# Optimization experiments

Measured on AMD Instinct MI355X. Metric: run time of the kernel, lower is better.

The kernel has to match this reference:

```python
import jax, jax.numpy as jnp
import numpy as np


def setup_inputs() -> dict:
    key = jax.random.key(0)
    k1, k2, k3 = jax.random.split(key, 3)
    x = jax.random.normal(k1, (8, 256, 160, 160), dtype=jnp.float32)
    # conv weights: OIHW layout, Kaiming-ish scale
    w7 = jax.random.normal(k2, (1, 2, 7, 7), dtype=jnp.float32) * (1.0 / np.sqrt(2 * 7 * 7))
    w3 = jax.random.normal(k3, (1, 2, 3, 3), dtype=jnp.float32) * (1.0 / np.sqrt(2 * 3 * 3))
    alpha = jnp.asarray(0.5, dtype=jnp.float32)
    return {"x": x, "w7": w7, "w3": w3, "alpha": alpha}


def _conv_same(desc, w, pad):
    # desc: [B, 2, H, W], w: [1, 2, k, k] -> [B, 1, H, W]
    return jax.lax.conv_general_dilated(
        desc, w, window_strides=(1, 1), padding=[(pad, pad), (pad, pad)],
        dimension_numbers=("NCHW", "OIHW", "NCHW"))


def reference(x, w7, w3, alpha):
    avg = jnp.mean(x, axis=1, keepdims=True)          # [B,1,H,W]
    mx = jnp.max(x, axis=1, keepdims=True)            # [B,1,H,W]
    desc = jnp.concatenate([avg, mx], axis=1)         # [B,2,H,W]
    a7 = _conv_same(desc, w7, 3)
    a3 = _conv_same(desc, w3, 1)
    w = jax.nn.sigmoid(alpha * a7 + (1.0 - alpha) * a3)
    return x * w
```

## Files before the change

kernel.cpp:

```cpp
#include <hip/hip_runtime.h>
#include <float.h>
#include <math.h>

#define Bn 8
#define Cn 256
#define Hn 160
#define Wn 160
#define HWn (Hn * Wn)
#define NPIX (Bn * HWn)
#define NTOT (Bn * Cn * HWn)
#define PBLK 256
#define BLKS (NPIX / PBLK)
#define BPB  (HWn / PBLK)

typedef float v4f __attribute__((ext_vector_type(4)));

__global__ __launch_bounds__(256) void k_reduce(const float* __restrict__ x,
                                                float* __restrict__ avgp,
                                                float* __restrict__ maxp) {
    const int tid  = threadIdx.x;
    const int lane = tid & 63;
    const int wv   = tid >> 6;
    const int base = blockIdx.x << 8;
    const int b    = base / HWn;
    const int hwb  = base - b * HWn;
    const float* xp = x + (size_t)b * Cn * HWn + hwb + (lane << 2);
    const int c0 = wv << 6;

    float4 s = make_float4(0.f, 0.f, 0.f, 0.f);
    float4 m = make_float4(-FLT_MAX, -FLT_MAX, -FLT_MAX, -FLT_MAX);
    #pragma unroll 8
    for (int c = 0; c < 64; ++c) {
        const float4 v = *reinterpret_cast<const float4*>(xp + (size_t)(c0 + c) * HWn);
        s.x += v.x; s.y += v.y; s.z += v.z; s.w += v.w;
        m.x = fmaxf(m.x, v.x); m.y = fmaxf(m.y, v.y);
        m.z = fmaxf(m.z, v.z); m.w = fmaxf(m.w, v.w);
    }

    __shared__ float4 ss[4][64];
    __shared__ float4 sm[4][64];
    ss[wv][lane] = s;
    sm[wv][lane] = m;
    __syncthreads();

    if (tid < 64) {
        const float4 s0 = ss[0][tid], s1 = ss[1][tid], s2 = ss[2][tid], s3 = ss[3][tid];
        const float4 m0 = sm[0][tid], m1 = sm[1][tid], m2 = sm[2][tid], m3 = sm[3][tid];
        const float inv = 1.0f / (float)Cn;
        float4 av, mx;
        av.x = (s0.x + s1.x + s2.x + s3.x) * inv;
        av.y = (s0.y + s1.y + s2.y + s3.y) * inv;
        av.z = (s0.z + s1.z + s2.z + s3.z) * inv;
        av.w = (s0.w + s1.w + s2.w + s3.w) * inv;
        mx.x = fmaxf(fmaxf(m0.x, m1.x), fmaxf(m2.x, m3.x));
        mx.y = fmaxf(fmaxf(m0.y, m1.y), fmaxf(m2.y, m3.y));
        mx.z = fmaxf(fmaxf(m0.z, m1.z), fmaxf(m2.z, m3.z));
        mx.w = fmaxf(fmaxf(m0.w, m1.w), fmaxf(m2.w, m3.w));
        reinterpret_cast<float4*>(avgp)[(base >> 2) + tid] = av;
        reinterpret_cast<float4*>(maxp)[(base >> 2) + tid] = mx;
    }
}

__global__ __launch_bounds__(256) void k_convmul(const float* __restrict__ x,
                                                 const float* __restrict__ avgp,
                                                 const float* __restrict__ maxp,
                                                 const float* __restrict__ w7,
                                                 const float* __restrict__ w3,
                                                 const float* __restrict__ alphap,
                                                 float* __restrict__ out) {
    __shared__ float w_lds[PBLK];

    const int tid  = threadIdx.x;
    const int base = blockIdx.x << 8;
    const int b    = base / HWn;
    const int hwb  = base - b * HWn;

    {
        const int hw = hwb + tid;
        const int h  = hw / Wn;
        const int w  = hw - h * Wn;
        const float* ap = avgp + b * HWn;
        const float* mp = maxp + b * HWn;

        float a7 = 0.f;
        #pragma unroll
        for (int kh = 0; kh < 7; ++kh) {
            const int hh = h + kh - 3;
            if (hh < 0 || hh >= Hn) continue;
            #pragma unroll
            for (int kw = 0; kw < 7; ++kw) {
                const int ww = w + kw - 3;
                if (ww < 0 || ww >= Wn) continue;
                const int o = hh * Wn + ww;
                a7 = fmaf(ap[o], w7[kh * 7 + kw], a7);
                a7 = fmaf(mp[o], w7[49 + kh * 7 + kw], a7);
            }
        }

        float a3 = 0.f;
        #pragma unroll
        for (int kh = 0; kh < 3; ++kh) {
            const int hh = h + kh - 1;
            if (hh < 0 || hh >= Hn) continue;
            #pragma unroll
            for (int kw = 0; kw < 3; ++kw) {
                const int ww = w + kw - 1;
                if (ww < 0 || ww >= Wn) continue;
                const int o = hh * Wn + ww;
                a3 = fmaf(ap[o], w3[kh * 3 + kw], a3);
                a3 = fmaf(mp[o], w3[9 + kh * 3 + kw], a3);
            }
        }

        const float alpha = *alphap;
        const float z = alpha * a7 + (1.0f - alpha) * a3;
        w_lds[tid] = 1.0f / (1.0f + expf(-z));
    }
    __syncthreads();

    const int lane = tid & 63;
    const int wv   = tid >> 6;
    const int c0   = wv << 6;

    const float4 wf = reinterpret_cast<const float4*>(w_lds)[lane];
    const v4f wvf = { wf.x, wf.y, wf.z, wf.w };

    const size_t off0 = (size_t)b * Cn * HWn + hwb + (lane << 2);
    const v4f* __restrict__ xin = reinterpret_cast<const v4f*>(x + off0);
    v4f* __restrict__ oout = reinterpret_cast<v4f*>(out + off0);

    #pragma unroll 8
    for (int c = 0; c < 64; ++c) {
        const size_t idx = ((size_t)(c0 + c) * HWn) >> 2;
        const v4f xv = __builtin_nontemporal_load(xin + idx);
        __builtin_nontemporal_store(xv * wvf, oout + idx);
    }
}

extern "C" void kernel_launch(void* const* d_in, const int* in_sizes, int n_in,
                              void* d_out, int out_size, void* d_ws, size_t ws_size,
                              hipStream_t stream) {
    const float* x      = (const float*)d_in[0];
    const float* w7     = (const float*)d_in[1];
    const float* w3     = (const float*)d_in[2];
    const float* alphap = (const float*)d_in[3];
    float* out = (float*)d_out;

    float* avgp = (float*)d_ws;
    float* maxp = avgp + NPIX;

    k_reduce <<<BLKS, 256, 0, stream>>>(x, avgp, maxp);
    k_convmul<<<BLKS, 256, 0, stream>>>(x, avgp, maxp, w7, w3, alphap, out);
}
```

Baseline: 114.9 us.

## Fuse channel reduction and conv-multiply into one cooperative kernel with grid sync

The two kernels become a single cooperative kernel. Each block first reduces its pixel tile over channels, then waits at a grid-wide barrier, then computes the 7x7/3x3 conv and sigmoid and scales x. The aim is to drop the second kernel launch and its gap, and to re-read each block's x slice while it may still sit in the large last-level cache, so the x load is now a normal load instead of a nontemporal one. In exchange, all 800 blocks must be co-resident for the cooperative launch to work. The grid barrier adds a global synchronisation point that serialises the two phases across the whole device.

```diff
diff --git a/kernel.cpp b/kernel.cpp
--- a/kernel.cpp
+++ b/kernel.cpp
@@ -1,6 +1,9 @@
 #include <hip/hip_runtime.h>
+#include <hip/hip_cooperative_groups.h>
 #include <float.h>
 #include <math.h>
+
+namespace cg = cooperative_groups;
 
 #define Bn 8
 #define Cn 256
@@ -8,73 +11,67 @@
 #define Wn 160
 #define HWn (Hn * Wn)
 #define NPIX (Bn * HWn)
-#define NTOT (Bn * Cn * HWn)
 #define PBLK 256
 #define BLKS (NPIX / PBLK)
-#define BPB  (HWn / PBLK)
 
 typedef float v4f __attribute__((ext_vector_type(4)));
 
-__global__ __launch_bounds__(256) void k_reduce(const float* __restrict__ x,
-                                                float* __restrict__ avgp,
-                                                float* __restrict__ maxp) {
+__global__ __launch_bounds__(256) void k_fused(const float* __restrict__ x,
+                                               const float* __restrict__ w7,
+                                               const float* __restrict__ w3,
+                                               const float* __restrict__ alphap,
+                                               float* __restrict__ avgp,
+                                               float* __restrict__ maxp,
+                                               float* __restrict__ out) {
     const int tid  = threadIdx.x;
     const int lane = tid & 63;
     const int wv   = tid >> 6;
     const int base = blockIdx.x << 8;
     const int b    = base / HWn;
     const int hwb  = base - b * HWn;
-    const float* xp = x + (size_t)b * Cn * HWn + hwb + (lane << 2);
-    const int c0 = wv << 6;
+    const int c0   = wv << 6;
+    const size_t off0 = (size_t)b * Cn * HWn + hwb + (lane << 2);
 
-    float4 s = make_float4(0.f, 0.f, 0.f, 0.f);
-    float4 m = make_float4(-FLT_MAX, -FLT_MAX, -FLT_MAX, -FLT_MAX);
-    #pragma unroll 8
-    for (int c = 0; c < 64; ++c) {
-        const float4 v = *reinterpret_cast<const float4*>(xp + (size_t)(c0 + c) * HWn);
-        s.x += v.x; s.y += v.y; s.z += v.z; s.w += v.w;
-        m.x = fmaxf(m.x, v.x); m.y = fmaxf(m.y, v.y);
-        m.z = fmaxf(m.z, v.z); m.w = fmaxf(m.w, v.w);
+    {
+        const float* xp = x + off0;
+        float4 s = make_float4(0.f, 0.f, 0.f, 0.f);
+        float4 m = make_float4(-FLT_MAX, -FLT_MAX, -FLT_MAX, -FLT_MAX);
+        #pragma unroll 8
+        for (int c = 0; c < 64; ++c) {
+            const float4 v = *reinterpret_cast<const float4*>(xp + (size_t)(c0 + c) * HWn);
+            s.x += v.x; s.y += v.y; s.z += v.z; s.w += v.w;
+            m.x = fmaxf(m.x, v.x); m.y = fmaxf(m.y, v.y);
+            m.z = fmaxf(m.z, v.z); m.w = fmaxf(m.w, v.w);
+        }
+
+        __shared__ float4 ss[4][64];
+        __shared__ float4 sm[4][64];
+        ss[wv][lane] = s;
+        sm[wv][lane] = m;
+        __syncthreads();
+
+        if (tid < 64) {
+            const float4 s0 = ss[0][tid], s1 = ss[1][tid], s2 = ss[2][tid], s3 = ss[3][tid];
+            const float4 m0 = sm[0][tid], m1 = sm[1][tid], m2 = sm[2][tid], m3 = sm[3][tid];
+            const float inv = 1.0f / (float)Cn;
+            float4 av, mx;
+            av.x = (s0.x + s1.x + s2.x + s3.x) * inv;
+            av.y = (s0.y + s1.y + s2.y + s3.y) * inv;
+            av.z = (s0.z + s1.z + s2.z + s3.z) * inv;
+            av.w = (s0.w + s1.w + s2.w + s3.w) * inv;
+            mx.x = fmaxf(fmaxf(m0.x, m1.x), fmaxf(m2.x, m3.x));
+            mx.y = fmaxf(fmaxf(m0.y, m1.y), fmaxf(m2.y, m3.y));
+            mx.z = fmaxf(fmaxf(m0.z, m1.z), fmaxf(m2.z, m3.z));
+            mx.w = fmaxf(fmaxf(m0.w, m1.w), fmaxf(m2.w, m3.w));
+            reinterpret_cast<float4*>(avgp)[(base >> 2) + tid] = av;
+            reinterpret_cast<float4*>(maxp)[(base >> 2) + tid] = mx;
+        }
     }
 
-    __shared__ float4 ss[4][64];
-    __shared__ float4 sm[4][64];
-    ss[wv][lane] = s;
-    sm[wv][lane] = m;
-    __syncthreads();
+    __threadfence();
+    cg::this_grid().sync();
 
-    if (tid < 64) {
-        const float4 s0 = ss[0][tid], s1 = ss[1][tid], s2 = ss[2][tid], s3 = ss[3][tid];
-        const float4 m0 = sm[0][tid], m1 = sm[1][tid], m2 = sm[2][tid], m3 = sm[3][tid];
-        const float inv = 1.0f / (float)Cn;
-        float4 av, mx;
-        av.x = (s0.x + s1.x + s2.x + s3.x) * inv;
-        av.y = (s0.y + s1.y + s2.y + s3.y) * inv;
-        av.z = (s0.z + s1.z + s2.z + s3.z) * inv;
-        av.w = (s0.w + s1.w + s2.w + s3.w) * inv;
-        mx.x = fmaxf(fmaxf(m0.x, m1.x), fmaxf(m2.x, m3.x));
-        mx.y = fmaxf(fmaxf(m0.y, m1.y), fmaxf(m2.y, m3.y));
-        mx.z = fmaxf(fmaxf(m0.z, m1.z), fmaxf(m2.z, m3.z));
-        mx.w = fmaxf(fmaxf(m0.w, m1.w), fmaxf(m2.w, m3.w));
-        reinterpret_cast<float4*>(avgp)[(base >> 2) + tid] = av;
-        reinterpret_cast<float4*>(maxp)[(base >> 2) + tid] = mx;
-    }
-}
-
-__global__ __launch_bounds__(256) void k_convmul(const float* __restrict__ x,
-                                                 const float* __restrict__ avgp,
-                                                 const float* __restrict__ maxp,
-                                                 const float* __restrict__ w7,
-                                                 const float* __restrict__ w3,
-                                                 const float* __restrict__ alphap,
-                                                 float* __restrict__ out) {
     __shared__ float w_lds[PBLK];
-
-    const int tid  = threadIdx.x;
-    const int base = blockIdx.x << 8;
-    const int b    = base / HWn;
-    const int hwb  = base - b * HWn;
-
     {
         const int hw = hwb + tid;
         const int h  = hw / Wn;
@@ -118,22 +115,18 @@
     }
     __syncthreads();
 
-    const int lane = tid & 63;
-    const int wv   = tid >> 6;
-    const int c0   = wv << 6;
+    {
+        const float4 wf = reinterpret_cast<const float4*>(w_lds)[lane];
+        const v4f wvf = { wf.x, wf.y, wf.z, wf.w };
+        const v4f* __restrict__ xin = reinterpret_cast<const v4f*>(x + off0);
+        v4f* __restrict__ oout = reinterpret_cast<v4f*>(out + off0);
 
-    const float4 wf = reinterpret_cast<const float4*>(w_lds)[lane];
-    const v4f wvf = { wf.x, wf.y, wf.z, wf.w };
-
-    const size_t off0 = (size_t)b * Cn * HWn + hwb + (lane << 2);
-    const v4f* __restrict__ xin = reinterpret_cast<const v4f*>(x + off0);
-    v4f* __restrict__ oout = reinterpret_cast<v4f*>(out + off0);
-
-    #pragma unroll 8
-    for (int c = 0; c < 64; ++c) {
-        const size_t idx = ((size_t)(c0 + c) * HWn) >> 2;
-        const v4f xv = __builtin_nontemporal_load(xin + idx);
-        __builtin_nontemporal_store(xv * wvf, oout + idx);
+        #pragma unroll 8
+        for (int c = 0; c < 64; ++c) {
+            const size_t idx = ((size_t)(c0 + c) * HWn) >> 2;
+            const v4f xv = xin[idx];
+            __builtin_nontemporal_store(xv * wvf, oout + idx);
+        }
     }
 }
 
@@ -149,6 +142,8 @@
     float* avgp = (float*)d_ws;
     float* maxp = avgp + NPIX;
 
-    k_reduce <<<BLKS, 256, 0, stream>>>(x, avgp, maxp);
-    k_convmul<<<BLKS, 256, 0, stream>>>(x, avgp, maxp, w7, w3, alphap, out);
+    void* args[] = { (void*)&x, (void*)&w7, (void*)&w3, (void*)&alphap,
+                     (void*)&avgp, (void*)&maxp, (void*)&out };
+    hipLaunchCooperativeKernel((const void*)k_fused,
+                               dim3(BLKS), dim3(256), args, 0, stream);
 }
```

New measurement: 296.7 us. 158% more time.

## Split channel reduction and separate conv from broadcast multiply for more parallelism

Applied to the files above, without the earlier changes.

The channel reduction now runs as two channel halves per pixel block, doubling the grid and writing partial sums and maxima. A new conv kernel combines the partials, stages the needed avg/max rows in LDS and writes a sigmoid weight map. A separate multiply kernel uses 128-pixel blocks, doubling its grid, and reads x with ordinary loads instead of nontemporal loads. The aim is better latency hiding on a bandwidth-bound workload, at the cost of an extra launch and extra workspace traffic.

```diff
diff --git a/kernel.cpp b/kernel.cpp
--- a/kernel.cpp
+++ b/kernel.cpp
@@ -9,28 +9,27 @@
 #define HWn (Hn * Wn)
 #define NPIX (Bn * HWn)
 #define NTOT (Bn * Cn * HWn)
-#define PBLK 256
-#define BLKS (NPIX / PBLK)
-#define BPB  (HWn / PBLK)
 
 typedef float v4f __attribute__((ext_vector_type(4)));
 
 __global__ __launch_bounds__(256) void k_reduce(const float* __restrict__ x,
-                                                float* __restrict__ avgp,
-                                                float* __restrict__ maxp) {
+                                                float* __restrict__ psum,
+                                                float* __restrict__ pmax) {
     const int tid  = threadIdx.x;
     const int lane = tid & 63;
     const int wv   = tid >> 6;
-    const int base = blockIdx.x << 8;
+    const int pb   = blockIdx.x >> 1;
+    const int half = blockIdx.x & 1;
+    const int base = pb << 8;
     const int b    = base / HWn;
     const int hwb  = base - b * HWn;
     const float* xp = x + (size_t)b * Cn * HWn + hwb + (lane << 2);
-    const int c0 = wv << 6;
+    const int c0 = (half << 7) + (wv << 5);
 
     float4 s = make_float4(0.f, 0.f, 0.f, 0.f);
     float4 m = make_float4(-FLT_MAX, -FLT_MAX, -FLT_MAX, -FLT_MAX);
-    #pragma unroll 8
-    for (int c = 0; c < 64; ++c) {
+    #pragma unroll 16
+    for (int c = 0; c < 32; ++c) {
         const float4 v = *reinterpret_cast<const float4*>(xp + (size_t)(c0 + c) * HWn);
         s.x += v.x; s.y += v.y; s.z += v.z; s.w += v.w;
         m.x = fmaxf(m.x, v.x); m.y = fmaxf(m.y, v.y);
@@ -46,54 +45,78 @@
     if (tid < 64) {
         const float4 s0 = ss[0][tid], s1 = ss[1][tid], s2 = ss[2][tid], s3 = ss[3][tid];
         const float4 m0 = sm[0][tid], m1 = sm[1][tid], m2 = sm[2][tid], m3 = sm[3][tid];
-        const float inv = 1.0f / (float)Cn;
-        float4 av, mx;
-        av.x = (s0.x + s1.x + s2.x + s3.x) * inv;
-        av.y = (s0.y + s1.y + s2.y + s3.y) * inv;
-        av.z = (s0.z + s1.z + s2.z + s3.z) * inv;
-        av.w = (s0.w + s1.w + s2.w + s3.w) * inv;
-        mx.x = fmaxf(fmaxf(m0.x, m1.x), fmaxf(m2.x, m3.x));
-        mx.y = fmaxf(fmaxf(m0.y, m1.y), fmaxf(m2.y, m3.y));
-        mx.z = fmaxf(fmaxf(m0.z, m1.z), fmaxf(m2.z, m3.z));
-        mx.w = fmaxf(fmaxf(m0.w, m1.w), fmaxf(m2.w, m3.w));
-        reinterpret_cast<float4*>(avgp)[(base >> 2) + tid] = av;
-        reinterpret_cast<float4*>(maxp)[(base >> 2) + tid] = mx;
+        float4 as, am;
+        as.x = (s0.x + s1.x) + (s2.x + s3.x);
+        as.y = (s0.y + s1.y) + (s2.y + s3.y);
+        as.z = (s0.z + s1.z) + (s2.z + s3.z);
+        as.w = (s0.w + s1.w) + (s2.w + s3.w);
+        am.x = fmaxf(fmaxf(m0.x, m1.x), fmaxf(m2.x, m3.x));
+        am.y = fmaxf(fmaxf(m0.y, m1.y), fmaxf(m2.y, m3.y));
+        am.z = fmaxf(fmaxf(m0.z, m1.z), fmaxf(m2.z, m3.z));
+        am.w = fmaxf(fmaxf(m0.w, m1.w), fmaxf(m2.w, m3.w));
+        reinterpret_cast<float4*>(psum + (size_t)half * NPIX)[(base >> 2) + tid] = as;
+        reinterpret_cast<float4*>(pmax + (size_t)half * NPIX)[(base >> 2) + tid] = am;
     }
 }
 
-__global__ __launch_bounds__(256) void k_convmul(const float* __restrict__ x,
-                                                 const float* __restrict__ avgp,
-                                                 const float* __restrict__ maxp,
-                                                 const float* __restrict__ w7,
-                                                 const float* __restrict__ w3,
-                                                 const float* __restrict__ alphap,
-                                                 float* __restrict__ out) {
-    __shared__ float w_lds[PBLK];
+__global__ __launch_bounds__(256) void k_conv(const float* __restrict__ psum,
+                                              const float* __restrict__ pmax,
+                                              const float* __restrict__ w7,
+                                              const float* __restrict__ w3,
+                                              const float* __restrict__ alphap,
+                                              float* __restrict__ wmap) {
+    __shared__ float shmem[2880];
+    __shared__ float dummy_pad;
 
     const int tid  = threadIdx.x;
     const int base = blockIdx.x << 8;
     const int b    = base / HWn;
     const int hwb  = base - b * HWn;
 
+    const int r0 = hwb / Wn;
+    const int rl = (hwb + 255) / Wn;
+    const int rs = (r0 - 3 < 0) ? 0 : r0 - 3;
+    const int re = (rl + 3 > Hn - 1) ? Hn - 1 : rl + 3;
+    const int nrows = re - rs + 1;
+    const int prow  = nrows * Wn;
+
+    {
+        const size_t bofs = (size_t)b * HWn + rs * Wn;
+        const float* s0 = psum + bofs;
+        const float* s1 = psum + NPIX + bofs;
+        const float* m0 = pmax + bofs;
+        const float* m1 = pmax + NPIX + bofs;
+        const float inv = 1.0f / (float)Cn;
+        const int total = 2 * prow;
+        for (int idx = tid; idx < total; idx += 256) {
+            if (idx < prow) {
+                shmem[idx] = (s0[idx] + s1[idx]) * inv;
+            } else {
+                const int o = idx - prow;
+                shmem[idx] = fmaxf(m0[o], m1[o]);
+            }
+        }
+    }
+    __syncthreads();
+
     {
         const int hw = hwb + tid;
         const int h  = hw / Wn;
         const int w  = hw - h * Wn;
-        const float* ap = avgp + b * HWn;
-        const float* mp = maxp + b * HWn;
 
         float a7 = 0.f;
         #pragma unroll
         for (int kh = 0; kh < 7; ++kh) {
             const int hh = h + kh - 3;
             if (hh < 0 || hh >= Hn) continue;
+            const float* arow = &shmem[(hh - rs) * Wn];
+            const float* mrow = arow + prow;
             #pragma unroll
             for (int kw = 0; kw < 7; ++kw) {
                 const int ww = w + kw - 3;
                 if (ww < 0 || ww >= Wn) continue;
-                const int o = hh * Wn + ww;
-                a7 = fmaf(ap[o], w7[kh * 7 + kw], a7);
-                a7 = fmaf(mp[o], w7[49 + kh * 7 + kw], a7);
+                a7 = fmaf(arow[ww], w7[kh * 7 + kw], a7);
+                a7 = fmaf(mrow[ww], w7[49 + kh * 7 + kw], a7);
             }
         }
 
@@ -102,37 +125,46 @@
         for (int kh = 0; kh < 3; ++kh) {
             const int hh = h + kh - 1;
             if (hh < 0 || hh >= Hn) continue;
+            const float* arow = &shmem[(hh - rs) * Wn];
+            const float* mrow = arow + prow;
             #pragma unroll
             for (int kw = 0; kw < 3; ++kw) {
                 const int ww = w + kw - 1;
                 if (ww < 0 || ww >= Wn) continue;
-                const int o = hh * Wn + ww;
-                a3 = fmaf(ap[o], w3[kh * 3 + kw], a3);
-                a3 = fmaf(mp[o], w3[9 + kh * 3 + kw], a3);
+                a3 = fmaf(arow[ww], w3[kh * 3 + kw], a3);
+                a3 = fmaf(mrow[ww], w3[9 + kh * 3 + kw], a3);
             }
         }
 
         const float alpha = *alphap;
         const float z = alpha * a7 + (1.0f - alpha) * a3;
-        w_lds[tid] = 1.0f / (1.0f + expf(-z));
+        wmap[base + tid] = 1.0f / (1.0f + expf(-z));
+        (void)dummy_pad;
     }
-    __syncthreads();
+}
 
-    const int lane = tid & 63;
-    const int wv   = tid >> 6;
-    const int c0   = wv << 6;
+__global__ __launch_bounds__(256) void k_mul(const float* __restrict__ x,
+                                             const float* __restrict__ wmap,
+                                             float* __restrict__ out) {
+    const int tid  = threadIdx.x;
+    const int g    = tid & 31;
+    const int cs   = tid >> 5;
+    const int base = blockIdx.x << 7;
+    const int b    = base / HWn;
+    const int hwb  = base - b * HWn;
 
-    const float4 wf = reinterpret_cast<const float4*>(w_lds)[lane];
+    const float4 wf = reinterpret_cast<const float4*>(wmap)[(base >> 2) + g];
     const v4f wvf = { wf.x, wf.y, wf.z, wf.w };
 
-    const size_t off0 = (size_t)b * Cn * HWn + hwb + (lane << 2);
+    const size_t off0 = (size_t)b * Cn * HWn + hwb + (g << 2);
     const v4f* __restrict__ xin = reinterpret_cast<const v4f*>(x + off0);
     v4f* __restrict__ oout = reinterpret_cast<v4f*>(out + off0);
+    const int c0 = cs << 5;
 
     #pragma unroll 8
-    for (int c = 0; c < 64; ++c) {
-        const size_t idx = ((size_t)(c0 + c) * HWn) >> 2;
-        const v4f xv = __builtin_nontemporal_load(xin + idx);
+    for (int k = 0; k < 32; ++k) {
+        const size_t idx = (size_t)(c0 + k) * (HWn / 4);
+        const v4f xv = xin[idx];
         __builtin_nontemporal_store(xv * wvf, oout + idx);
     }
 }
@@ -146,9 +178,11 @@
     const float* alphap = (const float*)d_in[3];
     float* out = (float*)d_out;
 
-    float* avgp = (float*)d_ws;
-    float* maxp = avgp + NPIX;
+    float* psum = (float*)d_ws;
+    float* pmax = psum + 2 * NPIX;
+    float* wmap = pmax + 2 * NPIX;
 
-    k_reduce <<<BLKS, 256, 0, stream>>>(x, avgp, maxp);
-    k_convmul<<<BLKS, 256, 0, stream>>>(x, avgp, maxp, w7, w3, alphap, out);
+    k_reduce<<<1600, 256, 0, stream>>>(x, psum, pmax);
+    k_conv  <<<800,  256, 0, stream>>>(psum, pmax, w7, w3, alphap, wmap);
+    k_mul   <<<1600, 256, 0, stream>>>(x, wmap, out);
 }
```

Measured after the change: 108.7 us. 1.06x faster.
